# Kernel tuning notes

Measured on AMD Instinct MI355X. Metric: run time of the kernel, lower is better.

The kernel has to match this reference:

```python
import jax, jax.numpy as jnp
import numpy as np

B, L, D = 16, 1024, 512
EPS = 1e-6


def setup_inputs() -> dict:
    key = jax.random.key(0)
    ks = jax.random.split(key, 12)
    inp = {
        'q': jax.random.normal(ks[0], (B, L, D), jnp.float32),
        'k': jax.random.normal(ks[1], (B, L, D), jnp.float32),
        'v': jax.random.normal(ks[2], (B, L, D), jnp.float32),
        'inputs_lengths': jax.random.randint(ks[3], (B,), 1, L + 1),
        'distance_matrix': jax.random.uniform(ks[4], (B, L, L), jnp.float32),
        'Wq': jax.random.normal(ks[5], (D, D), jnp.float32) / np.sqrt(D),
        'Wk': jax.random.normal(ks[6], (D, D), jnp.float32) / np.sqrt(D),
        'Wv': jax.random.normal(ks[7], (D, D), jnp.float32) / np.sqrt(D),
        'Wqt': jax.random.normal(ks[8], (D, D), jnp.float32) / np.sqrt(D),
        'Wkt': jax.random.normal(ks[9], (D, D), jnp.float32) / np.sqrt(D),
        'Wfc': jax.random.normal(ks[10], (D, D), jnp.float32) / np.sqrt(D),
        'gamma': jnp.ones((D,), jnp.float32),
        'beta': jnp.zeros((D,), jnp.float32),
    }
    return inp


def reference(q, k, v, inputs_lengths, distance_matrix, Wq, Wk, Wv, Wqt, Wkt, Wfc, gamma, beta):
    temperature = jnp.asarray(D, q.dtype) ** 0.5
    residual = q
    # projections (torch Linear: x @ W.T)
    qp = jnp.einsum('bld,ed->ble', q, Wq)
    kp = jnp.einsum('bld,ed->ble', k, Wk)
    vp = jnp.einsum('bld,ed->ble', v, Wv)
    qt = jnp.einsum('bld,ed->ble', q, Wqt)
    kt = jnp.einsum('bld,ed->ble', k, Wkt)
    # distance-weighted time features: [B,L,L] @ [B,L,D]
    qt = jnp.einsum('blm,bmd->bld', distance_matrix, qt)
    kt = jnp.einsum('blm,bmd->bld', distance_matrix, kt)
    # scores: content + distance term
    attn = jnp.einsum('bld,bmd->blm', qp / temperature, kp)
    attn = attn + jnp.einsum('bld,bmd->blm', qt / temperature, kt)
    # pad_zero_masking: zero out key positions beyond each sequence length
    mask = (jnp.arange(L)[None, :] < inputs_lengths[:, None]).astype(attn.dtype)  # [B, L]
    mask = mask[:, None, :]  # [B, 1, L] broadcast over query dim
    attn = jnp.tanh(attn * mask) * mask
    out = jnp.einsum('blm,bmd->bld', attn, vp)
    out = jnp.einsum('bld,ed->ble', out, Wfc) + residual
    # LayerNorm(eps=1e-6)
    mu = jnp.mean(out, axis=-1, keepdims=True)
    var = jnp.mean((out - mu) ** 2, axis=-1, keepdims=True)
    out = (out - mu) * jax.lax.rsqrt(var + EPS) * gamma + beta
    return (out, attn)
```

## Files before the change

### kernel.cpp

```cpp
#include <hip/hip_runtime.h>
#include <math.h>

#define LL 1024
#define DD 512
#define NB 16

typedef __attribute__((ext_vector_type(8))) short bf16x8;
typedef __attribute__((ext_vector_type(4))) float f32x4;
typedef unsigned short u16;
typedef unsigned int u32;
typedef const __attribute__((address_space(1))) void* gptr_t;
typedef __attribute__((address_space(3))) void* sptr_t;

static const long NLD = (long)NB * LL * DD;
static const long NLL = (long)NB * LL * LL;

__device__ __forceinline__ u16 f2bf(float x) {
  u32 u = __float_as_uint(x);
  u += 0x7fffu + ((u >> 16) & 1u);
  return (u16)(u >> 16);
}
__device__ __forceinline__ float bf2f(u16 h) {
  return __uint_as_float((u32)h << 16);
}

__global__ __launch_bounds__(256) void k_split3(
    const float* __restrict__ q, const float* __restrict__ k,
    const float* __restrict__ v, u16* __restrict__ qh, u16* __restrict__ ql,
    u16* __restrict__ kh, u16* __restrict__ kl, u16* __restrict__ vh) {
  const int z = blockIdx.z;
  const float* x = (z == 0) ? q : (z == 1) ? k : v;
  u16* hi = (z == 0) ? qh : (z == 1) ? kh : vh;
  u16* lo = (z == 0) ? ql : kl;
  const long stride = (long)gridDim.x * 1024;
  for (long i = ((long)blockIdx.x * 256 + threadIdx.x) * 4; i < NLD;
       i += stride) {
    const float4 vv = *(const float4*)(x + i);
    ushort4 h;
    h.x = f2bf(vv.x);
    h.y = f2bf(vv.y);
    h.z = f2bf(vv.z);
    h.w = f2bf(vv.w);
    *(ushort4*)(hi + i) = h;
    if (z < 2) {
      ushort4 s;
      s.x = f2bf(vv.x - bf2f(h.x));
      s.y = f2bf(vv.y - bf2f(h.y));
      s.z = f2bf(vv.z - bf2f(h.z));
      s.w = f2bf(vv.w - bf2f(h.w));
      *(ushort4*)(lo + i) = s;
    }
  }
}

__global__ __launch_bounds__(256) void k_splitd(const float* __restrict__ x,
                                                u16* __restrict__ hi,
                                                u16* __restrict__ lo) {
  const long stride = (long)gridDim.x * 1024;
  for (long i = ((long)blockIdx.x * 256 + threadIdx.x) * 4; i < NLL;
       i += stride) {
    const float4 v = *(const float4*)(x + i);
    ushort4 h, s;
    h.x = f2bf(v.x);
    h.y = f2bf(v.y);
    h.z = f2bf(v.z);
    h.w = f2bf(v.w);
    s.x = f2bf(v.x - bf2f(h.x));
    s.y = f2bf(v.y - bf2f(h.y));
    s.z = f2bf(v.z - bf2f(h.z));
    s.w = f2bf(v.w - bf2f(h.w));
    *(ushort4*)(hi + i) = h;
    *(ushort4*)(lo + i) = s;
  }
}

__global__ __launch_bounds__(256) void k_splitw(
    const float* __restrict__ Wq, const float* __restrict__ Wk,
    const float* __restrict__ Wv, const float* __restrict__ Wfc,
    const float* __restrict__ Wqt, const float* __restrict__ Wkt,
    u16* __restrict__ Wq_h, u16* __restrict__ Wk_h, u16* __restrict__ Wv_h,
    u16* __restrict__ Wfc_h, u16* __restrict__ Wqt_h,
    u16* __restrict__ Wqt_l, u16* __restrict__ Wkt_h,
    u16* __restrict__ Wkt_l) {
  const int z = blockIdx.z;
  const float* x;
  u16 *hi, *lo = nullptr;
  switch (z) {
    case 0: x = Wq; hi = Wq_h; break;
    case 1: x = Wk; hi = Wk_h; break;
    case 2: x = Wv; hi = Wv_h; break;
    case 3: x = Wfc; hi = Wfc_h; break;
    case 4: x = Wqt; hi = Wqt_h; lo = Wqt_l; break;
    default: x = Wkt; hi = Wkt_h; lo = Wkt_l; break;
  }
  const long i = ((long)blockIdx.x * 256 + threadIdx.x) * 4;
  const float4 v = *(const float4*)(x + i);
  ushort4 h;
  h.x = f2bf(v.x);
  h.y = f2bf(v.y);
  h.z = f2bf(v.z);
  h.w = f2bf(v.w);
  *(ushort4*)(hi + i) = h;
  if (z >= 4) {
    ushort4 s;
    s.x = f2bf(v.x - bf2f(h.x));
    s.y = f2bf(v.y - bf2f(h.y));
    s.z = f2bf(v.z - bf2f(h.z));
    s.w = f2bf(v.w - bf2f(h.w));
    *(ushort4*)(lo + i) = s;
  }
}

template <int NISS>
__device__ __forceinline__ void stage_tile(const u16* __restrict__ G, long ld,
                                           int row0, int k0, char* lds, int w,
                                           int l) {
#pragma unroll
  for (int i = 0; i < NISS; ++i) {
    const int off = i * 4096 + w * 1024 + l * 16;
    const int r = off >> 6;
    const int cp = (off >> 4) & 3;
    const int c = cp ^ ((r >> 1) & 3);
    __builtin_amdgcn_global_load_lds(
        (gptr_t)(G + (long)(row0 + r) * ld + k0 + c * 8),
        (sptr_t)(lds + i * 4096 + w * 1024), 16, 0, 0);
  }
}

__device__ __forceinline__ bf16x8 read_frag(const char* lds, int r, int ks) {
  const int cp = ks ^ ((r >> 1) & 3);
  return *(const bf16x8*)(lds + r * 64 + cp * 16);
}

__device__ __forceinline__ void core_plain(const u16* __restrict__ A, long lda,
                                           const u16* __restrict__ B, long ldb,
                                           int K, int bm, int bn, char* smem,
                                           f32x4 acc[4][4]) {
  const int tid = threadIdx.x, w = tid >> 6, l = tid & 63;
  const int wm = (w >> 1) * 64, wn = (w & 1) * 64;
  const int fr = l & 15, ks = l >> 4;
  char* As = smem;
  char* Bs = smem + 8192;
  for (int k0 = 0; k0 < K; k0 += 32) {
    stage_tile<2>(A, lda, bm, k0, As, w, l);
    stage_tile<2>(B, ldb, bn, k0, Bs, w, l);
    __syncthreads();
    bf16x8 af[4], bg[4];
#pragma unroll
    for (int i = 0; i < 4; ++i) {
      af[i] = read_frag(As, wm + i * 16 + fr, ks);
      bg[i] = read_frag(Bs, wn + i * 16 + fr, ks);
    }
#pragma unroll
    for (int mi = 0; mi < 4; ++mi)
#pragma unroll
      for (int ni = 0; ni < 4; ++ni)
        acc[mi][ni] = __builtin_amdgcn_mfma_f32_16x16x32_bf16(
            af[mi], bg[ni], acc[mi][ni], 0, 0, 0);
    __syncthreads();
  }
}

__device__ __forceinline__ void core_split(
    const u16* __restrict__ Ah, const u16* __restrict__ Al, long lda,
    const u16* __restrict__ Bh, const u16* __restrict__ Bl, long ldb, int K,
    int bm, int bn, char* smem, f32x4 acc[4][4]) {
  const int tid = threadIdx.x, w = tid >> 6, l = tid & 63;
  const int wm = (w >> 1) * 64, wn = (w & 1) * 64;
  const int fr = l & 15, ks = l >> 4;
  char* Ash = smem;
  char* Bsh = smem + 8192;
  char* Asl = smem + 16384;
  char* Bsl = smem + 24576;
  for (int k0 = 0; k0 < K; k0 += 32) {
    stage_tile<2>(Ah, lda, bm, k0, Ash, w, l);
    stage_tile<2>(Bh, ldb, bn, k0, Bsh, w, l);
    stage_tile<2>(Al, lda, bm, k0, Asl, w, l);
    stage_tile<2>(Bl, ldb, bn, k0, Bsl, w, l);
    __syncthreads();
    bf16x8 ah[4], bh[4];
#pragma unroll
    for (int i = 0; i < 4; ++i) {
      ah[i] = read_frag(Ash, wm + i * 16 + fr, ks);
      bh[i] = read_frag(Bsh, wn + i * 16 + fr, ks);
    }
#pragma unroll
    for (int mi = 0; mi < 4; ++mi)
#pragma unroll
      for (int ni = 0; ni < 4; ++ni)
        acc[mi][ni] = __builtin_amdgcn_mfma_f32_16x16x32_bf16(
            ah[mi], bh[ni], acc[mi][ni], 0, 0, 0);
    bf16x8 bl[4];
#pragma unroll
    for (int ni = 0; ni < 4; ++ni)
      bl[ni] = read_frag(Bsl, wn + ni * 16 + fr, ks);
#pragma unroll
    for (int mi = 0; mi < 4; ++mi)
#pragma unroll
      for (int ni = 0; ni < 4; ++ni)
        acc[mi][ni] = __builtin_amdgcn_mfma_f32_16x16x32_bf16(
            ah[mi], bl[ni], acc[mi][ni], 0, 0, 0);
    bf16x8 al[4];
#pragma unroll
    for (int mi = 0; mi < 4; ++mi)
      al[mi] = read_frag(Asl, wm + mi * 16 + fr, ks);
#pragma unroll
    for (int mi = 0; mi < 4; ++mi)
#pragma unroll
      for (int ni = 0; ni < 4; ++ni)
        acc[mi][ni] = __builtin_amdgcn_mfma_f32_16x16x32_bf16(
            al[mi], bh[ni], acc[mi][ni], 0, 0, 0);
    __syncthreads();
  }
}

#define EPI_PROLOG()                                       \
  const int tid = threadIdx.x, w = tid >> 6, l = tid & 63; \
  const int wm = (w >> 1) * 64, wn = (w & 1) * 64;         \
  const int fr = l & 15, ks = l >> 4;

__device__ __forceinline__ int scan_batches(const int* __restrict__ lens,
                                            int e, int mult, int* loc,
                                            int* rem) {
  for (int i = 0; i < NB; ++i) {
    const int c = mult * ((lens[i] + 127) >> 7);
    if (e < c) {
      *loc = e;
      return i;
    }
    e -= c;
  }
  *rem = e;
  return -1;
}

__global__ __launch_bounds__(256, 3) void k_proj_p(
    const u16* __restrict__ q_hi, const u16* __restrict__ k_hi,
    const u16* __restrict__ v_hi, const u16* __restrict__ Wq_h,
    const u16* __restrict__ Wk_h, const u16* __restrict__ Wv_h,
    const int* __restrict__ lens, u16* __restrict__ qp, u16* __restrict__ kp,
    u16* __restrict__ vp) {
  const int flat = blockIdx.x;
  const u16 *A, *B;
  u16* C;
  int bm, bn;
  if (flat < 512) {
    A = q_hi;
    B = Wq_h;
    C = qp;
    bm = (flat >> 2) * 128;
    bn = (flat & 3) * 128;
  } else {
    int loc, rem;
    int b = scan_batches(lens, flat - 512, 4, &loc, &rem);
    if (b >= 0) {
      A = k_hi;
      B = Wk_h;
      C = kp;
    } else {
      b = scan_batches(lens, rem, 4, &loc, &rem);
      if (b < 0) return;
      A = v_hi;
      B = Wv_h;
      C = vp;
    }
    bm = b * 1024 + (loc >> 2) * 128;
    bn = (loc & 3) * 128;
  }
  __shared__ __align__(16) char smem[16384];
  f32x4 acc[4][4] = {};
  core_plain(A, DD, B, DD, DD, bm, bn, smem, acc);
  EPI_PROLOG()
#pragma unroll
  for (int mi = 0; mi < 4; ++mi) {
    const int R0 = bm + wm + mi * 16 + ks * 4;
#pragma unroll
    for (int ni = 0; ni < 4; ++ni) {
      const int col = bn + wn + ni * 16 + fr;
#pragma unroll
      for (int j = 0; j < 4; ++j)
        C[(long)(R0 + j) * DD + col] = f2bf(acc[mi][ni][j]);
    }
  }
}

__global__ __launch_bounds__(256, 3) void k_proj_t(
    const u16* __restrict__ q_hi, const u16* __restrict__ q_lo,
    const u16* __restrict__ k_hi, const u16* __restrict__ k_lo,
    const u16* __restrict__ Wqt_h, const u16* __restrict__ Wqt_l,
    const u16* __restrict__ Wkt_h, const u16* __restrict__ Wkt_l,
    u16* __restrict__ qt0h, u16* __restrict__ qt0l, u16* __restrict__ kt0h,
    u16* __restrict__ kt0l) {
  const int sel = blockIdx.z;
  const u16* Ah = sel ? k_hi : q_hi;
  const u16* Al = sel ? k_lo : q_lo;
  const u16* Bh = sel ? Wkt_h : Wqt_h;
  const u16* Bl = sel ? Wkt_l : Wqt_l;
  u16* Ch = sel ? kt0h : qt0h;
  u16* Cl = sel ? kt0l : qt0l;
  __shared__ __align__(16) char smem[32768];
  const int bm = blockIdx.y * 128, bn = blockIdx.x * 128;
  f32x4 acc[4][4] = {};
  core_split(Ah, Al, DD, Bh, Bl, DD, DD, bm, bn, smem, acc);
  EPI_PROLOG()
#pragma unroll
  for (int mi = 0; mi < 4; ++mi) {
    const int R0 = bm + wm + mi * 16 + ks * 4;
#pragma unroll
    for (int ni = 0; ni < 4; ++ni) {
      const int col = bn + wn + ni * 16 + fr;
#pragma unroll
      for (int j = 0; j < 4; ++j) {
        const long idx = (long)(R0 + j) * DD + col;
        const float x = acc[mi][ni][j];
        const u16 h = f2bf(x);
        Ch[idx] = h;
        Cl[idx] = f2bf(x - bf2f(h));
      }
    }
  }
}

__global__ __launch_bounds__(256) void k_tr(
    const u16* __restrict__ qt0h, const u16* __restrict__ qt0l,
    const u16* __restrict__ kt0h, const u16* __restrict__ kt0l,
    const u16* __restrict__ vp, const int* __restrict__ lens,
    u16* __restrict__ qTh, u16* __restrict__ qTl, u16* __restrict__ kTh,
    u16* __restrict__ kTl, u16* __restrict__ vpT) {
  const int z = blockIdx.z;
  const int b = z / 5, s = z - b * 5;
  const int r0 = blockIdx.y * 64, c0 = blockIdx.x * 64;
  if (s == 4 && r0 >= lens[b]) return;
  const u16* X;
  u16* O;
  switch (s) {
    case 0: X = qt0h; O = qTh; break;
    case 1: X = qt0l; O = qTl; break;
    case 2: X = kt0h; O = kTh; break;
    case 3: X = kt0l; O = kTl; break;
    default: X = vp; O = vpT; break;
  }
  X += (long)b * LL * DD;
  O += (long)b * LL * DD;
  __shared__ u16 t[64][68];
  const int tid = threadIdx.x;
#pragma unroll
  for (int i = 0; i < 16; ++i) {
    const int idx = tid + i * 256;
    t[idx >> 6][idx & 63] = X[(long)(r0 + (idx >> 6)) * DD + c0 + (idx & 63)];
  }
  __syncthreads();
#pragma unroll
  for (int i = 0; i < 16; ++i) {
    const int idx = tid + i * 256;
    const int rr = idx >> 6, cc = idx & 63;
    O[(long)(c0 + rr) * LL + r0 + cc] = t[cc][rr];
  }
}

__global__ __launch_bounds__(256, 3) void k_dist_g(
    const u16* __restrict__ dist_h, const u16* __restrict__ dist_l,
    const u16* __restrict__ qT_h, const u16* __restrict__ qT_l,
    const u16* __restrict__ kT_h, const u16* __restrict__ kT_l,
    const int* __restrict__ lens, u16* __restrict__ qt_h,
    u16* __restrict__ qt_l, u16* __restrict__ kt_h, u16* __restrict__ kt_l) {
  const int flat = blockIdx.x;
  int b, sel, bm, bn;
  if (flat < 512) {
    sel = 0;
    b = flat & 15;
    const int r = flat >> 4;
    bm = (r >> 2) * 128;
    bn = (r & 3) * 128;
  } else {
    int loc, rem;
    b = scan_batches(lens, flat - 512, 4, &loc, &rem);
    if (b < 0) return;
    sel = 1;
    bm = (loc >> 2) * 128;
    bn = (loc & 3) * 128;
  }
  const u16* Ah = dist_h + (long)b * LL * LL;
  const u16* Al = dist_l + (long)b * LL * LL;
  const u16* Bh = (sel ? kT_h : qT_h) + (long)b * LL * DD;
  const u16* Bl = (sel ? kT_l : qT_l) + (long)b * LL * DD;
  u16* Oh = (sel ? kt_h : qt_h) + (long)b * LL * DD;
  u16* Ol = (sel ? kt_l : qt_l) + (long)b * LL * DD;
  __shared__ __align__(16) char smem[32768];
  f32x4 acc[4][4] = {};
  core_split(Ah, Al, LL, Bh, Bl, LL, LL, bm, bn, smem, acc);
  EPI_PROLOG()
#pragma unroll
  for (int mi = 0; mi < 4; ++mi) {
    const int R0 = bm + wm + mi * 16 + ks * 4;
#pragma unroll
    for (int ni = 0; ni < 4; ++ni) {
      const int col = bn + wn + ni * 16 + fr;
#pragma unroll
      for (int j = 0; j < 4; ++j) {
        const long idx = (long)(R0 + j) * DD + col;
        const float x = acc[mi][ni][j];
        const u16 h = f2bf(x);
        Oh[idx] = h;
        Ol[idx] = f2bf(x - bf2f(h));
      }
    }
  }
}

__global__ __launch_bounds__(256, 3) void k_score(
    const u16* __restrict__ qp, const u16* __restrict__ kp,
    const u16* __restrict__ qt_h, const u16* __restrict__ qt_l,
    const u16* __restrict__ kt_h, const u16* __restrict__ kt_l,
    const int* __restrict__ lens, float* __restrict__ attnF,
    u16* __restrict__ attnB) {
  const int tid = threadIdx.x;
  int loc, rem;
  int b = scan_batches(lens, blockIdx.x, 8, &loc, &rem);
  int bm, bn;
  if (b < 0) {
    for (int i = 0; i < NB; ++i) {
      const int nbn = (lens[i] + 127) >> 7;
      const int c = (8 - nbn) << 3;
      if (rem < c) {
        b = i;
        const int wdt = 8 - nbn;
        bm = (rem / wdt) * 128;
        bn = (nbn + rem % wdt) * 128;
        break;
      }
      rem -= c;
    }
    if (b < 0) return;
    const long baseF = (long)b * LL * LL;
    const float4 zf = make_float4(0.f, 0.f, 0.f, 0.f);
    const ushort4 zh = {0, 0, 0, 0};
    for (int i = tid; i < 4096; i += 256) {
      const int row = i >> 5, c = (i & 31) << 2;
      const long idx = baseF + (long)(bm + row) * LL + bn + c;
      *(float4*)&attnF[idx] = zf;
      *(ushort4*)&attnB[idx] = zh;
    }
    return;
  }
  const int nbn = (lens[b] + 127) >> 7;
  bm = (loc / nbn) * 128;
  bn = (loc % nbn) * 128;
  const int len = lens[b];
  const long baseF = (long)b * LL * LL;
  const long od = (long)b * LL * DD;
  const u16* Ah = qt_h + od;
  const u16* Al = qt_l + od;
  const u16* Bh = kt_h + od;
  const u16* Bl = kt_l + od;
  const u16* Ap = qp + od;
  const u16* Bp = kp + od;
  __shared__ __align__(16) char smem[49152];
  char* Ash = smem;
  char* Bsh = smem + 8192;
  char* Asl = smem + 16384;
  char* Bsl = smem + 24576;
  char* Aps = smem + 32768;
  char* Bps = smem + 40960;
  const int w = tid >> 6, l = tid & 63;
  const int wm = (w >> 1) * 64, wn = (w & 1) * 64;
  const int fr = l & 15, ks = l >> 4;
  f32x4 acc[4][4] = {};
  for (int k0 = 0; k0 < DD; k0 += 32) {
    stage_tile<2>(Ah, DD, bm, k0, Ash, w, l);
    stage_tile<2>(Bh, DD, bn, k0, Bsh, w, l);
    stage_tile<2>(Al, DD, bm, k0, Asl, w, l);
    stage_tile<2>(Bl, DD, bn, k0, Bsl, w, l);
    stage_tile<2>(Ap, DD, bm, k0, Aps, w, l);
    stage_tile<2>(Bp, DD, bn, k0, Bps, w, l);
    __syncthreads();
    bf16x8 ah[4], bh[4];
#pragma unroll
    for (int i = 0; i < 4; ++i) {
      ah[i] = read_frag(Ash, wm + i * 16 + fr, ks);
      bh[i] = read_frag(Bsh, wn + i * 16 + fr, ks);
    }
#pragma unroll
    for (int mi = 0; mi < 4; ++mi)
#pragma unroll
      for (int ni = 0; ni < 4; ++ni)
        acc[mi][ni] = __builtin_amdgcn_mfma_f32_16x16x32_bf16(
            ah[mi], bh[ni], acc[mi][ni], 0, 0, 0);
    bf16x8 bl[4];
#pragma unroll
    for (int ni = 0; ni < 4; ++ni)
      bl[ni] = read_frag(Bsl, wn + ni * 16 + fr, ks);
#pragma unroll
    for (int mi = 0; mi < 4; ++mi)
#pragma unroll
      for (int ni = 0; ni < 4; ++ni)
        acc[mi][ni] = __builtin_amdgcn_mfma_f32_16x16x32_bf16(
            ah[mi], bl[ni], acc[mi][ni], 0, 0, 0);
    bf16x8 al[4];
#pragma unroll
    for (int mi = 0; mi < 4; ++mi)
      al[mi] = read_frag(Asl, wm + mi * 16 + fr, ks);
#pragma unroll
    for (int mi = 0; mi < 4; ++mi)
#pragma unroll
      for (int ni = 0; ni < 4; ++ni)
        acc[mi][ni] = __builtin_amdgcn_mfma_f32_16x16x32_bf16(
            al[mi], bh[ni], acc[mi][ni], 0, 0, 0);
    bf16x8 ap[4], bp[4];
#pragma unroll
    for (int i = 0; i < 4; ++i) {
      ap[i] = read_frag(Aps, wm + i * 16 + fr, ks);
      bp[i] = read_frag(Bps, wn + i * 16 + fr, ks);
    }
#pragma unroll
    for (int mi = 0; mi < 4; ++mi)
#pragma unroll
      for (int ni = 0; ni < 4; ++ni)
        acc[mi][ni] = __builtin_amdgcn_mfma_f32_16x16x32_bf16(
            ap[mi], bp[ni], acc[mi][ni], 0, 0, 0);
    __syncthreads();
  }
  const float invt = 0.04419417382415922f;
#pragma unroll
  for (int mi = 0; mi < 4; ++mi) {
    const int R0 = bm + wm + mi * 16 + ks * 4;
#pragma unroll
    for (int ni = 0; ni < 4; ++ni) {
      const int col = bn + wn + ni * 16 + fr;
      const float m = (col < len) ? 1.0f : 0.0f;
#pragma unroll
      for (int j = 0; j < 4; ++j) {
        const float s = tanhf(acc[mi][ni][j] * invt * m) * m;
        const long idx = baseF + (long)(R0 + j) * LL + col;
        attnF[idx] = s;
        attnB[idx] = f2bf(s);
      }
    }
  }
}

__global__ __launch_bounds__(256, 3) void k_pv(const u16* __restrict__ attnB,
                                               const u16* __restrict__ vpT,
                                               const int* __restrict__ lens,
                                               u16* __restrict__ out0) {
  const int flat = blockIdx.x;
  const int b = flat & 15;
  const int r = flat >> 4;
  const int bm = (r >> 2) * 128, bn = (r & 3) * 128;
  const int Kt = ((lens[b] + 31) >> 5) << 5;
  __shared__ __align__(16) char smem[16384];
  f32x4 acc[4][4] = {};
  core_plain(attnB + (long)b * LL * LL, LL, vpT + (long)b * LL * DD, LL, Kt,
             bm, bn, smem, acc);
  u16* C = out0 + (long)b * LL * DD;
  EPI_PROLOG()
#pragma unroll
  for (int mi = 0; mi < 4; ++mi) {
    const int R0 = bm + wm + mi * 16 + ks * 4;
#pragma unroll
    for (int ni = 0; ni < 4; ++ni) {
      const int col = bn + wn + ni * 16 + fr;
#pragma unroll
      for (int j = 0; j < 4; ++j)
        C[(long)(R0 + j) * DD + col] = f2bf(acc[mi][ni][j]);
    }
  }
}

__global__ __launch_bounds__(256, 2) void k_fcln(
    const u16* __restrict__ out0, const u16* __restrict__ Wfc_h,
    const float* __restrict__ q, const float* __restrict__ gamma,
    const float* __restrict__ beta, float* __restrict__ outO) {
  __shared__ __align__(16) char smem[36864];
  __shared__ float red[2][64][5];
  const int tid = threadIdx.x, w = tid >> 6, l = tid & 63;
  const int wn = w * 128;
  const int fr = l & 15, ks = l >> 4;
  const int bm = blockIdx.x * 64;
  char* As = smem;
  char* Bs = smem + 4096;
  f32x4 acc[4][8] = {};
  for (int k0 = 0; k0 < DD; k0 += 32) {
    stage_tile<1>(out0, DD, bm, k0, As, w, l);
    stage_tile<8>(Wfc_h, DD, 0, k0, Bs, w, l);
    __syncthreads();
    bf16x8 af[4], bg[8];
#pragma unroll
    for (int mi = 0; mi < 4; ++mi) af[mi] = read_frag(As, mi * 16 + fr, ks);
#pragma unroll
    for (int ni = 0; ni < 8; ++ni)
      bg[ni] = read_frag(Bs, wn + ni * 16 + fr, ks);
#pragma unroll
    for (int mi = 0; mi < 4; ++mi)
#pragma unroll
      for (int ni = 0; ni < 8; ++ni)
        acc[mi][ni] = __builtin_amdgcn_mfma_f32_16x16x32_bf16(
            af[mi], bg[ni], acc[mi][ni], 0, 0, 0);
    __syncthreads();
  }
  float p1[4][4], p2[4][4];
#pragma unroll
  for (int mi = 0; mi < 4; ++mi)
#pragma unroll
    for (int j = 0; j < 4; ++j) {
      p1[mi][j] = 0.0f;
      p2[mi][j] = 0.0f;
    }
#pragma unroll
  for (int mi = 0; mi < 4; ++mi) {
    const int r = mi * 16 + ks * 4;
#pragma unroll
    for (int ni = 0; ni < 8; ++ni) {
      const int col = wn + ni * 16 + fr;
#pragma unroll
      for (int j = 0; j < 4; ++j) {
        const float val = acc[mi][ni][j] + q[(long)(bm + r + j) * DD + col];
        acc[mi][ni][j] = val;
        p1[mi][j] += val;
        p2[mi][j] += val * val;
      }
    }
  }
#pragma unroll
  for (int off = 1; off < 16; off <<= 1) {
#pragma unroll
    for (int mi = 0; mi < 4; ++mi)
#pragma unroll
      for (int j = 0; j < 4; ++j) {
        p1[mi][j] += __shfl_xor(p1[mi][j], off);
        p2[mi][j] += __shfl_xor(p2[mi][j], off);
      }
  }
  if (fr == 0) {
#pragma unroll
    for (int mi = 0; mi < 4; ++mi)
#pragma unroll
      for (int j = 0; j < 4; ++j) {
        red[0][mi * 16 + ks * 4 + j][w] = p1[mi][j];
        red[1][mi * 16 + ks * 4 + j][w] = p2[mi][j];
      }
  }
  __syncthreads();
#pragma unroll
  for (int mi = 0; mi < 4; ++mi) {
#pragma unroll
    for (int j = 0; j < 4; ++j) {
      const int r = mi * 16 + ks * 4 + j;
      const float s1 =
          red[0][r][0] + red[0][r][1] + red[0][r][2] + red[0][r][3];
      const float s2 =
          red[1][r][0] + red[1][r][1] + red[1][r][2] + red[1][r][3];
      const float mu = s1 * (1.0f / DD);
      const float rs = rsqrtf(s2 * (1.0f / DD) - mu * mu + 1e-6f);
#pragma unroll
      for (int ni = 0; ni < 8; ++ni) {
        const int col = wn + ni * 16 + fr;
        outO[(long)(bm + r) * DD + col] =
            (acc[mi][ni][j] - mu) * rs * gamma[col] + beta[col];
      }
    }
  }
}

extern "C" void kernel_launch(void* const* d_in, const int* in_sizes, int n_in,
                              void* d_out, int out_size, void* d_ws,
                              size_t ws_size, hipStream_t stream) {
  const float* q = (const float*)d_in[0];
  const float* k = (const float*)d_in[1];
  const float* v = (const float*)d_in[2];
  const int* lens = (const int*)d_in[3];
  const float* dist = (const float*)d_in[4];
  const float* Wq = (const float*)d_in[5];
  const float* Wk = (const float*)d_in[6];
  const float* Wv = (const float*)d_in[7];
  const float* Wqt = (const float*)d_in[8];
  const float* Wkt = (const float*)d_in[9];
  const float* Wfc = (const float*)d_in[10];
  const float* gamma = (const float*)d_in[11];
  const float* beta = (const float*)d_in[12];

  char* W = (char*)d_ws;
  const size_t SB = 16777216;
  u16* q_hi = (u16*)(W + 0 * SB);
  u16* q_lo = (u16*)(W + 1 * SB);
  u16* k_hi = (u16*)(W + 2 * SB);
  u16* k_lo = (u16*)(W + 3 * SB);
  u16* v_hi = (u16*)(W + 4 * SB);
  u16* dist_h = (u16*)(W + 5 * SB);
  u16* dist_l = (u16*)(W + 7 * SB);
  u16* qp_bf = (u16*)(W + 9 * SB);
  u16* kp_bf = (u16*)(W + 10 * SB);
  u16* vp_bf = (u16*)(W + 11 * SB);
  u16* qt0h = (u16*)(W + 12 * SB);
  u16* qt0l = (u16*)(W + 13 * SB);
  u16* kt0h = (u16*)(W + 14 * SB);
  u16* kt0l = (u16*)(W + 15 * SB);
  u16* qT_h = (u16*)(W + 16 * SB);
  u16* qT_l = (u16*)(W + 17 * SB);
  u16* kT_h = (u16*)(W + 18 * SB);
  u16* kT_l = (u16*)(W + 19 * SB);
  char* WB = W + 20 * SB;
  const size_t WS = 524288;
  u16* Wq_h = (u16*)(WB + 0 * WS);
  u16* Wk_h = (u16*)(WB + 1 * WS);
  u16* Wv_h = (u16*)(WB + 2 * WS);
  u16* Wfc_h = (u16*)(WB + 3 * WS);
  u16* Wqt_h = (u16*)(WB + 4 * WS);
  u16* Wqt_l = (u16*)(WB + 5 * WS);
  u16* Wkt_h = (u16*)(WB + 6 * WS);
  u16* Wkt_l = (u16*)(WB + 7 * WS);
  u16* qt_h = q_hi;
  u16* qt_l = q_lo;
  u16* kt_h = k_hi;
  u16* kt_l = k_lo;
  u16* vpT = v_hi;
  u16* attnB = dist_h;
  u16* out0 = qp_bf;

  float* outO = (float*)d_out;
  float* attnF = outO + NLD;

  dim3 blk(256);
  k_split3<<<dim3(1024, 1, 3), blk, 0, stream>>>(q, k, v, q_hi, q_lo, k_hi,
                                                 k_lo, v_hi);
  k_splitd<<<4096, blk, 0, stream>>>(dist, dist_h, dist_l);
  k_splitw<<<dim3(256, 1, 6), blk, 0, stream>>>(Wq, Wk, Wv, Wfc, Wqt, Wkt,
                                                Wq_h, Wk_h, Wv_h, Wfc_h,
                                                Wqt_h, Wqt_l, Wkt_h, Wkt_l);

  k_proj_p<<<1536, blk, 0, stream>>>(q_hi, k_hi, v_hi, Wq_h, Wk_h, Wv_h, lens,
                                     qp_bf, kp_bf, vp_bf);
  k_proj_t<<<dim3(4, 128, 2), blk, 0, stream>>>(q_hi, q_lo, k_hi, k_lo, Wqt_h,
                                                Wqt_l, Wkt_h, Wkt_l, qt0h,
                                                qt0l, kt0h, kt0l);
  k_tr<<<dim3(8, 16, 80), blk, 0, stream>>>(qt0h, qt0l, kt0h, kt0l, vp_bf,
                                            lens, qT_h, qT_l, kT_h, kT_l,
                                            vpT);
  k_dist_g<<<1024, blk, 0, stream>>>(dist_h, dist_l, qT_h, qT_l, kT_h, kT_l,
                                     lens, qt_h, qt_l, kt_h, kt_l);
  k_score<<<1024, blk, 0, stream>>>(qp_bf, kp_bf, qt_h, qt_l, kt_h, kt_l,
                                    lens, attnF, attnB);
  k_pv<<<512, blk, 0, stream>>>(attnB, vpT, lens, out0);
  k_fcln<<<256, blk, 0, stream>>>(out0, Wfc_h, q, gamma, beta, outO);
}
```

Before: 458.7 us.

## Remap block indices for XCD-aware locality in GEMM kernels

Adds an XCD-aware block index permutation so that consecutive logical tiles (chunks of 16) land on the same XCD, where they share an L2. It also reorders tile traversal so that blocks of the same batch, and grouped 4-row supertiles, run together and reuse A/B panels in cache. This targets L2 misses across MI355X's multiple chiplets. The remap assumes the grid size is a multiple of 128; otherwise the mapping may produce out-of-range or duplicated indices for tail blocks.

```diff
diff --git a/kernel.cpp b/kernel.cpp
--- a/kernel.cpp
+++ b/kernel.cpp
@@ -22,6 +22,11 @@
 }
 __device__ __forceinline__ float bf2f(u16 h) {
   return __uint_as_float((u32)h << 16);
+}
+
+__device__ __forceinline__ int xcd_chunk16(int flat) {
+  const int j = flat >> 3;
+  return ((j >> 4) << 7) + ((flat & 7) << 4) + (j & 15);
 }
 
 __global__ __launch_bounds__(256) void k_split3(
@@ -240,7 +245,7 @@
     const u16* __restrict__ Wk_h, const u16* __restrict__ Wv_h,
     const int* __restrict__ lens, u16* __restrict__ qp, u16* __restrict__ kp,
     u16* __restrict__ vp) {
-  const int flat = blockIdx.x;
+  const int flat = xcd_chunk16(blockIdx.x);
   const u16 *A, *B;
   u16* C;
   int bm, bn;
@@ -364,14 +369,15 @@
     const u16* __restrict__ kT_h, const u16* __restrict__ kT_l,
     const int* __restrict__ lens, u16* __restrict__ qt_h,
     u16* __restrict__ qt_l, u16* __restrict__ kt_h, u16* __restrict__ kt_l) {
-  const int flat = blockIdx.x;
+  const int flat = xcd_chunk16(blockIdx.x);
   int b, sel, bm, bn;
   if (flat < 512) {
     sel = 0;
-    b = flat & 15;
-    const int r = flat >> 4;
-    bm = (r >> 2) * 128;
-    bn = (r & 3) * 128;
+    b = flat >> 5;
+    const int r = flat & 31;
+    const int s = r >> 4, inner = r & 15;
+    bm = (s * 4 + (inner & 3)) * 128;
+    bn = (inner >> 2) * 128;
   } else {
     int loc, rem;
     b = scan_batches(lens, flat - 512, 4, &loc, &rem);
@@ -416,7 +422,7 @@
     u16* __restrict__ attnB) {
   const int tid = threadIdx.x;
   int loc, rem;
-  int b = scan_batches(lens, blockIdx.x, 8, &loc, &rem);
+  int b = scan_batches(lens, xcd_chunk16(blockIdx.x), 8, &loc, &rem);
   int bm, bn;
   if (b < 0) {
     for (int i = 0; i < NB; ++i) {
@@ -444,8 +450,12 @@
     return;
   }
   const int nbn = (lens[b] + 127) >> 7;
-  bm = (loc / nbn) * 128;
-  bn = (loc % nbn) * 128;
+  {
+    const int S = nbn << 2;
+    const int s = loc / S, inner = loc - s * S;
+    bm = (s * 4 + (inner & 3)) * 128;
+    bn = (inner >> 2) * 128;
+  }
   const int len = lens[b];
   const long baseF = (long)b * LL * LL;
   const long od = (long)b * LL * DD;
@@ -543,9 +553,9 @@
                                                const u16* __restrict__ vpT,
                                                const int* __restrict__ lens,
                                                u16* __restrict__ out0) {
-  const int flat = blockIdx.x;
-  const int b = flat & 15;
-  const int r = flat >> 4;
+  const int flat = xcd_chunk16(blockIdx.x);
+  const int b = flat >> 5;
+  const int r = flat & 31;
   const int bm = (r >> 2) * 128, bn = (r & 3) * 128;
   const int Kt = ((lens[b] + 31) >> 5) << 5;
   __shared__ __align__(16) char smem[16384];
```

After: 425.1 us. -7.3%, faster.
